# Kernel optimization log

Measured on AMD Instinct MI355X. Metric: run time of the kernel, lower is better.

## Reference

```python
import jax, jax.numpy as jnp
import numpy as np
from jax import lax

M, N, Q = 256, 65536, 64
LAMBDA_STAR = 0.1
LAMBDA_O = 0.1
T_ITERS = 16
PM_ITERS = 100


def setup_inputs() -> dict:
    key = jax.random.key(0)
    kx, kd = jax.random.split(key)
    X = jax.random.normal(kx, (M, N), dtype=jnp.float32)
    D = jax.random.normal(kd, (M, Q), dtype=jnp.float32)
    return {"X": X, "D": D}


def _power_method(D):
    # Largest eigenvalue of D^T D via 100-step power iteration (fixed random init).
    x0 = jax.random.normal(jax.random.key(1), (1, Q), dtype=D.dtype)

    def step(x, _):
        x = (x @ D.T) @ D          # [1,q] -> [1,m] -> [1,q]
        nm = jnp.linalg.norm(x)
        return x / nm, nm

    _, nms = lax.scan(step, x0, None, length=PM_ITERS)
    return nms[-1]


def reference(X, D):
    m, n = X.shape
    q = D.shape[1]
    alpha = _power_method(D)
    eta = 1.0 / alpha

    Iq = jnp.eye(q, dtype=D.dtype)
    Im = jnp.eye(m, dtype=D.dtype)
    top = jnp.concatenate([D.T @ D + LAMBDA_STAR * Iq, D.T], axis=1)   # [q, q+m]
    bot = jnp.concatenate([D, (1.0 + LAMBDA_STAR) * Im], axis=1)       # [m, q+m]
    H = jnp.eye(m + q, dtype=D.dtype) - eta * jnp.concatenate([top, bot], axis=0)
    W = eta * jnp.concatenate([D.T, Im], axis=0)                        # [(m+q), m]
    t = LAMBDA_O * eta * jnp.concatenate([jnp.zeros(q, D.dtype), jnp.ones(m, D.dtype)])

    b0 = W @ X                                                           # [(m+q), n]
    Z0 = jnp.zeros((m + q, n), dtype=X.dtype)

    def ista_step(carry, _):
        Z, b = carry
        Znew = jnp.maximum(0.0, b - t[:, None])    # thresholding (ger(t, ones) == t broadcast)
        b = b + H @ (Znew - Z)
        return (Znew, b), None

    (Z, _), _ = lax.scan(ista_step, (Z0, b0), None, length=T_ITERS)
    return Z
```

## Files before the change

kernel.cpp:

```cpp
#include <hip/hip_runtime.h>


typedef __bf16 bf16x8 __attribute__((ext_vector_type(8)));
typedef __bf16 bf16x2 __attribute__((ext_vector_type(2)));
typedef float f32x4 __attribute__((ext_vector_type(4)));
typedef float f32x2 __attribute__((ext_vector_type(2)));

#define MFMA16(a, b, c) __builtin_amdgcn_mfma_f32_16x16x32_bf16((a), (b), (c), 0, 0, 0)

#define NTOT 65536
#define NCOL 32

__device__ __forceinline__ unsigned pk2(float a, float b) {
#if __has_builtin(__builtin_amdgcn_cvt_pk_bf16_f32)
  return __builtin_bit_cast(unsigned, __builtin_amdgcn_cvt_pk_bf16_f32(a, b));
#else
  unsigned short ua = __builtin_bit_cast(unsigned short, (__bf16)a);
  unsigned short ub = __builtin_bit_cast(unsigned short, (__bf16)b);
  return (unsigned)ua | ((unsigned)ub << 16);
#endif
}
__device__ __forceinline__ unsigned pk2v(f32x2 v) { return pk2(v[0], v[1]); }
__device__ __forceinline__ f32x2 f2(float s) { f32x2 v = {s, s}; return v; }
__device__ __forceinline__ f32x2 pfma(f32x2 a, f32x2 b, f32x2 c) {
  return __builtin_elementwise_fma(a, b, c);
}
__device__ __forceinline__ f32x2 pmax0(f32x2 a) {
  return __builtin_elementwise_max(a, f2(0.f));
}

#define GOF(row) ((row) * 68 + (((row) >> 3) << 2))
__global__ void rnmf_prep(const float* __restrict__ D, void* __restrict__ ws) {
  float* wsf = (float*)ws;
  __bf16* Dbf = (__bf16*)((char*)ws + 256);
  __bf16* DTbf = (__bf16*)((char*)ws + 256 + 32768);

  __shared__ __bf16 DTl[64 * 264];
  __shared__ __bf16 gA[64 * 72];
  __shared__ __bf16 gB[64 * 72];
  __shared__ float gf[64 * 68 + 32];
  __shared__ __align__(16) float xv[64];

  const int tid = threadIdx.x;
  const int w = tid >> 6, lane = tid & 63, c = lane & 15, q4 = lane >> 4;

#pragma unroll
  for (int e = 0; e < 16; ++e) {
    int i4 = e * 256 + tid;
    float4 dv = *(const float4*)(D + i4 * 4);
    uint2 u; u.x = pk2(dv.x, dv.y); u.y = pk2(dv.z, dv.w);
    *(uint2*)(Dbf + i4 * 4) = u;
  }
#pragma unroll
  for (int e = 0; e < 64; ++e) {
    int flat = e * 256 + tid;
    int k = flat >> 6, a = flat & 63;
    DTl[a * 264 + k] = (__bf16)D[k * 64 + a];
  }
  __syncthreads();
#pragma unroll
  for (int e = 0; e < 8; ++e) {
    int fi = e * 256 + tid;
    int a = fi >> 5;
    int k = (fi * 8) & 255;
    *(bf16x8*)(DTbf + fi * 8) = *(const bf16x8*)&DTl[a * 264 + k];
  }
#pragma unroll
  for (int ct = 0; ct < 4; ++ct) {
    f32x4 acc = {0.f, 0.f, 0.f, 0.f};
#pragma unroll
    for (int kb = 0; kb < 8; ++kb) {
      bf16x8 a = *(const bf16x8*)&DTl[(16 * w + c) * 264 + 32 * kb + 8 * q4];
      bf16x8 b = *(const bf16x8*)&DTl[(16 * ct + c) * 264 + 32 * kb + 8 * q4];
      acc = MFMA16(a, b, acc);
    }
#pragma unroll
    for (int r = 0; r < 4; ++r)
      gA[(16 * w + 4 * q4 + r) * 72 + 16 * ct + c] = (__bf16)acc[r];
  }
  __syncthreads();
#pragma unroll
  for (int ct = 0; ct < 4; ++ct) {
    f32x4 acc = {0.f, 0.f, 0.f, 0.f};
#pragma unroll
    for (int kb = 0; kb < 2; ++kb) {
      bf16x8 a = *(const bf16x8*)&gA[(16 * w + c) * 72 + 32 * kb + 8 * q4];
      bf16x8 b = *(const bf16x8*)&gA[(16 * ct + c) * 72 + 32 * kb + 8 * q4];
      acc = MFMA16(a, b, acc);
    }
#pragma unroll
    for (int r = 0; r < 4; ++r)
      gB[(16 * w + 4 * q4 + r) * 72 + 16 * ct + c] = (__bf16)acc[r];
  }
  __syncthreads();
#pragma unroll
  for (int ct = 0; ct < 4; ++ct) {
    f32x4 acc = {0.f, 0.f, 0.f, 0.f};
#pragma unroll
    for (int kb = 0; kb < 2; ++kb) {
      bf16x8 a = *(const bf16x8*)&gB[(16 * w + c) * 72 + 32 * kb + 8 * q4];
      bf16x8 b = *(const bf16x8*)&gB[(16 * ct + c) * 72 + 32 * kb + 8 * q4];
      acc = MFMA16(a, b, acc);
    }
#pragma unroll
    for (int r = 0; r < 4; ++r)
      gA[(16 * w + 4 * q4 + r) * 72 + 16 * ct + c] = (__bf16)acc[r];
  }
  __syncthreads();
#pragma unroll
  for (int ct = 0; ct < 4; ++ct) {
    f32x4 acc = {0.f, 0.f, 0.f, 0.f};
#pragma unroll
    for (int kb = 0; kb < 2; ++kb) {
      bf16x8 a = *(const bf16x8*)&gA[(16 * w + c) * 72 + 32 * kb + 8 * q4];
      bf16x8 b = *(const bf16x8*)&gA[(16 * ct + c) * 72 + 32 * kb + 8 * q4];
      acc = MFMA16(a, b, acc);
    }
#pragma unroll
    for (int r = 0; r < 4; ++r)
      gf[GOF(16 * w + 4 * q4 + r) + 16 * ct + c] = acc[r];
  }
  __syncthreads();

  if (w == 0) {
    float td = gf[GOF(lane) + lane];
#pragma unroll
    for (int off = 32; off; off >>= 1) td += __shfl_xor(td, off, 64);
    const float tr = td;
    const float itr = 1.f / tr;
    xv[lane] = 1.f;
    float nm = 1.f;
    const int rowoff = GOF(lane);
    for (int itp = 0; itp < 28; ++itp) {
      float acc = 0.f;
#pragma unroll
      for (int k = 0; k < 64; k += 4) {
        float4 g = *(const float4*)&gf[rowoff + k];
        float4 xx = *(const float4*)&xv[k];
        acc = fmaf(g.x, xx.x, acc);
        acc = fmaf(g.y, xx.y, acc);
        acc = fmaf(g.z, xx.z, acc);
        acc = fmaf(g.w, xx.w, acc);
      }
      float y = acc * itr;
      float n2 = y * y;
#pragma unroll
      for (int off = 32; off; off >>= 1) n2 += __shfl_xor(n2, off, 64);
      nm = sqrtf(n2);
      xv[lane] = y / nm;
    }
    if (lane == 0) wsf[0] = 1.f / powf(nm * tr, 0.125f);
  }
}

__global__ __launch_bounds__(256, 3) void rnmf_main(const float* __restrict__ X,
                                                    float* __restrict__ Z,
                                                    const void* __restrict__ ws) {
  const float* wsf = (const float*)ws;
  const __bf16* Dbf = (const __bf16*)((const char*)ws + 256);
  const __bf16* DTbf = (const __bf16*)((const char*)ws + 256 + 32768);

  __shared__ __align__(16) char arena[33280];
  float* xs = (float*)arena;

  const int tid = threadIdx.x;
  const int w = tid >> 6;
  const int lane = tid & 63;
  const int c = lane & 15;
  const int q4 = lane >> 4;
  const int q4h = q4 >> 1, q4l = q4 & 1;
  const int j0 = blockIdx.x * NCOL;

#pragma unroll
  for (int e = 0; e < 8; ++e) {
    int idx = e * 256 + tid;
    int row = idx >> 3, c4 = (idx & 7) * 4;
    float4 g = *(const float4*)(X + row * NTOT + j0 + c4);
    xs[(c4 + 0) * 260 + row] = g.x;
    xs[(c4 + 1) * 260 + row] = g.y;
    xs[(c4 + 2) * 260 + row] = g.z;
    xs[(c4 + 3) * 260 + row] = g.w;
  }

  const float eta = wsf[0];
  const f32x2 etav = f2(eta);
  const f32x2 metav = f2(-eta);
  const f32x2 cqv = f2(1.f - 0.1f * eta);
  const f32x2 cmv = f2(1.f - 1.1f * eta);
  const float tm = 0.1f * eta;

  bf16x8 d1[4][2];
#pragma unroll
  for (int rt = 0; rt < 4; ++rt)
#pragma unroll
    for (int kb = 0; kb < 2; ++kb)
      d1[rt][kb] = *(const bf16x8*)(Dbf + (64 * w + 16 * rt + c) * 64 + 32 * kb + 8 * q4);
  bf16x8 d2[8];
#pragma unroll
  for (int kb = 0; kb < 8; ++kb)
    d2[kb] = *(const bf16x8*)(DTbf + (16 * w + c) * 256 + 32 * kb + 8 * q4);

  __syncthreads();

  f32x2 bqt2[2][2];
#pragma unroll
  for (int ct = 0; ct < 2; ++ct) {
    f32x4 acc = {0.f, 0.f, 0.f, 0.f};
#pragma unroll
    for (int kb = 0; kb < 8; ++kb) {
      const float* p = &xs[(16 * ct + c) * 260 + 32 * kb + 8 * q4];
      float4 lo = *(const float4*)p;
      float4 hi = *(const float4*)(p + 4);
      unsigned p0 = pk2(lo.x, lo.y), p1 = pk2(lo.z, lo.w);
      unsigned p2 = pk2(hi.x, hi.y), p3 = pk2(hi.z, hi.w);
      uint4 packed = {p0, p1, p2, p3};
      acc = MFMA16(d2[kb], __builtin_bit_cast(bf16x8, packed), acc);
    }
    f32x2 a0 = {acc[0], acc[1]}, a1 = {acc[2], acc[3]};
    bqt2[ct][0] = etav * a0;
    bqt2[ct][1] = etav * a1;
  }

  f32x2 bmt2[4][2][2];
#pragma unroll
  for (int rt = 0; rt < 4; ++rt)
#pragma unroll
    for (int ct = 0; ct < 2; ++ct) {
      const float* p = &xs[(16 * ct + c) * 260 + 64 * w + 16 * rt + 4 * q4];
      float4 v = *(const float4*)p;
      f32x2 x0 = {v.x, v.y}, x1 = {v.z, v.w};
      bmt2[rt][ct][0] = pfma(etav, x0, f2(-tm));
      bmt2[rt][ct][1] = pfma(etav, x1, f2(-tm));
    }

  __syncthreads();

  f32x2 zq2[2][2], zm2[4][2][2];
#pragma unroll
  for (int ct = 0; ct < 2; ++ct)
#pragma unroll
    for (int p = 0; p < 2; ++p) zq2[ct][p] = pmax0(bqt2[ct][p]);
#pragma unroll
  for (int rt = 0; rt < 4; ++rt)
#pragma unroll
    for (int ct = 0; ct < 2; ++ct)
#pragma unroll
      for (int p = 0; p < 2; ++p) zm2[rt][ct][p] = pmax0(bmt2[rt][ct][p]);

  char* smem = arena;
  const int rb = lane * 16;
  const int wzq = (w >> 1) * 1024 + ((2 * w) & 3) * 256 + q4h * 256 + c * 16 + 8 * q4l;
  const int wvb = 4096 + 2 * w * 1024 + q4h * 256 + c * 16 + 8 * q4l;

#pragma unroll
  for (int ct = 0; ct < 2; ++ct) {
    uint2 u; u.x = pk2v(zq2[ct][0]); u.y = pk2v(zq2[ct][1]);
    *(uint2*)(smem + wzq + ct * 2048) = u;
  }

  for (int it = 0; it < 15; ++it) {
    __syncthreads();
#pragma unroll
    for (int ct = 0; ct < 2; ++ct) {
      bf16x8 bz0 = *(const bf16x8*)(smem + rb + ct * 2048);
      bf16x8 bz1 = *(const bf16x8*)(smem + rb + ct * 2048 + 1024);
#pragma unroll
      for (int rt = 0; rt < 4; ++rt) {
        f32x4 acc = {0.f, 0.f, 0.f, 0.f};
        acc = MFMA16(d1[rt][0], bz0, acc);
        acc = MFMA16(d1[rt][1], bz1, acc);
        f32x2 u0 = {acc[0], acc[1]}, u1 = {acc[2], acc[3]};
        f32x2 z0 = zm2[rt][ct][0], z1 = zm2[rt][ct][1];
        f32x2 v0 = u0 + z0, v1 = u1 + z1;
        f32x2 t0 = pfma(cmv, z0, bmt2[rt][ct][0]);
        f32x2 t1 = pfma(cmv, z1, bmt2[rt][ct][1]);
        zm2[rt][ct][0] = pmax0(pfma(metav, u0, t0));
        zm2[rt][ct][1] = pmax0(pfma(metav, u1, t1));
        uint2 uu; uu.x = pk2v(v0); uu.y = pk2v(v1);
        *(uint2*)(smem + wvb + ct * 8192 + rt * 512) = uu;
      }
    }
    __syncthreads();
#pragma unroll
    for (int ct = 0; ct < 2; ++ct) {
      f32x4 acc = {0.f, 0.f, 0.f, 0.f};
#pragma unroll
      for (int kb = 0; kb < 8; ++kb) {
        bf16x8 bv = *(const bf16x8*)(smem + rb + 4096 + ct * 8192 + kb * 1024);
        acc = MFMA16(d2[kb], bv, acc);
      }
      f32x2 w0 = {acc[0], acc[1]}, w1 = {acc[2], acc[3]};
      f32x2 t0 = pfma(cqv, zq2[ct][0], bqt2[ct][0]);
      f32x2 t1 = pfma(cqv, zq2[ct][1], bqt2[ct][1]);
      zq2[ct][0] = pmax0(pfma(metav, w0, t0));
      zq2[ct][1] = pmax0(pfma(metav, w1, t1));
      uint2 u; u.x = pk2v(zq2[ct][0]); u.y = pk2v(zq2[ct][1]);
      *(uint2*)(smem + wzq + ct * 2048) = u;
    }
  }

#pragma unroll
  for (int ct = 0; ct < 2; ++ct)
#pragma unroll
    for (int p = 0; p < 2; ++p)
#pragma unroll
      for (int e = 0; e < 2; ++e)
        Z[(16 * w + 4 * q4 + 2 * p + e) * NTOT + j0 + 16 * ct + c] = zq2[ct][p][e];
#pragma unroll
  for (int rt = 0; rt < 4; ++rt)
#pragma unroll
    for (int ct = 0; ct < 2; ++ct)
#pragma unroll
      for (int p = 0; p < 2; ++p)
#pragma unroll
        for (int e = 0; e < 2; ++e)
          Z[(64 + 64 * w + 16 * rt + 4 * q4 + 2 * p + e) * NTOT + j0 + 16 * ct + c] = zm2[rt][ct][p][e];
}

extern "C" void kernel_launch(void* const* d_in, const int* in_sizes, int n_in,
                              void* d_out, int out_size, void* d_ws, size_t ws_size,
                              hipStream_t stream) {
  const float* X = (const float*)d_in[0];
  const float* D = (const float*)d_in[1];
  float* Z = (float*)d_out;
  rnmf_prep<<<dim3(1), dim3(256), 0, stream>>>(D, d_ws);
  rnmf_main<<<dim3(NTOT / NCOL), dim3(256), 0, stream>>>(X, Z, d_ws);
}
```

Baseline: 229.6 us.

## Stage X as bf16 in MFMA fragment layout to raise occupancy; rework power iteration

The main kernel now converts X to bf16 on load and stores it directly in the LDS layout the MFMA B-operand reads. This shrinks shared memory from 33280 to 20480 bytes, removes per-iteration packing, and drops one barrier. Launch bounds are raised from 3 to 5 blocks per CU to use the freed LDS. The prep kernel's power iteration now runs on all waves, skips per-step normalization, applies one rescale, and uses a Rayleigh quotient with fewer iterations. The trade-off is that the thresholded m-rows now start from bf16-rounded X rather than fp32, which costs some accuracy.

Measured after the change: 648.6 us. +182.5%, slower.

```diff
diff --git a/kernel.cpp b/kernel.cpp
--- a/kernel.cpp
+++ b/kernel.cpp
@@ -2,7 +2,7 @@
 
 
 typedef __bf16 bf16x8 __attribute__((ext_vector_type(8)));
-typedef __bf16 bf16x2 __attribute__((ext_vector_type(2)));
+typedef __bf16 bf16x4 __attribute__((ext_vector_type(4)));
 typedef float f32x4 __attribute__((ext_vector_type(4)));
 typedef float f32x2 __attribute__((ext_vector_type(2)));
 
@@ -29,7 +29,6 @@
   return __builtin_elementwise_max(a, f2(0.f));
 }
 
-#define GOF(row) ((row) * 68 + (((row) >> 3) << 2))
 __global__ void rnmf_prep(const float* __restrict__ D, void* __restrict__ ws) {
   float* wsf = (float*)ws;
   __bf16* Dbf = (__bf16*)((char*)ws + 256);
@@ -38,8 +37,8 @@
   __shared__ __bf16 DTl[64 * 264];
   __shared__ __bf16 gA[64 * 72];
   __shared__ __bf16 gB[64 * 72];
-  __shared__ float gf[64 * 68 + 32];
-  __shared__ __align__(16) float xv[64];
+  __shared__ float gf[64 * 68];
+  __shared__ __align__(16) float xv[2][64];
 
   const int tid = threadIdx.x;
   const int w = tid >> 6, lane = tid & 63, c = lane & 15, q4 = lane >> 4;
@@ -47,15 +46,14 @@
 #pragma unroll
   for (int e = 0; e < 16; ++e) {
     int i4 = e * 256 + tid;
+    int row = i4 >> 4, col4 = (i4 & 15) * 4;
     float4 dv = *(const float4*)(D + i4 * 4);
     uint2 u; u.x = pk2(dv.x, dv.y); u.y = pk2(dv.z, dv.w);
     *(uint2*)(Dbf + i4 * 4) = u;
-  }
-#pragma unroll
-  for (int e = 0; e < 64; ++e) {
-    int flat = e * 256 + tid;
-    int k = flat >> 6, a = flat & 63;
-    DTl[a * 264 + k] = (__bf16)D[k * 64 + a];
+    DTl[(col4 + 0) * 264 + row] = (__bf16)dv.x;
+    DTl[(col4 + 1) * 264 + row] = (__bf16)dv.y;
+    DTl[(col4 + 2) * 264 + row] = (__bf16)dv.z;
+    DTl[(col4 + 3) * 264 + row] = (__bf16)dv.w;
   }
   __syncthreads();
 #pragma unroll
@@ -118,50 +116,63 @@
     }
 #pragma unroll
     for (int r = 0; r < 4; ++r)
-      gf[GOF(16 * w + 4 * q4 + r) + 16 * ct + c] = acc[r];
-  }
-  __syncthreads();
-
-  if (w == 0) {
-    float td = gf[GOF(lane) + lane];
-#pragma unroll
-    for (int off = 32; off; off >>= 1) td += __shfl_xor(td, off, 64);
-    const float tr = td;
-    const float itr = 1.f / tr;
-    xv[lane] = 1.f;
-    float nm = 1.f;
-    const int rowoff = GOF(lane);
-    for (int itp = 0; itp < 28; ++itp) {
-      float acc = 0.f;
-#pragma unroll
-      for (int k = 0; k < 64; k += 4) {
-        float4 g = *(const float4*)&gf[rowoff + k];
-        float4 xx = *(const float4*)&xv[k];
-        acc = fmaf(g.x, xx.x, acc);
-        acc = fmaf(g.y, xx.y, acc);
-        acc = fmaf(g.z, xx.z, acc);
-        acc = fmaf(g.w, xx.w, acc);
-      }
-      float y = acc * itr;
-      float n2 = y * y;
-#pragma unroll
-      for (int off = 32; off; off >>= 1) n2 += __shfl_xor(n2, off, 64);
-      nm = sqrtf(n2);
-      xv[lane] = y / nm;
-    }
-    if (lane == 0) wsf[0] = 1.f / powf(nm * tr, 0.125f);
-  }
-}
-
-__global__ __launch_bounds__(256, 3) void rnmf_main(const float* __restrict__ X,
+      gf[(16 * w + 4 * q4 + r) * 68 + 16 * ct + c] = acc[r];
+  }
+  __syncthreads();
+
+  float td = gf[lane * 68 + lane];
+#pragma unroll
+  for (int off = 32; off; off >>= 1) td += __shfl_xor(td, off, 64);
+  const float tr = td;
+  const float itr = 1.f / tr;
+  const int rowoff = lane * 68;
+  float x = 1.f, xp = 1.f;
+  for (int itp = 0; itp < 17; ++itp) {
+    xv[itp & 1][lane] = x;
+    __syncthreads();
+    float a0 = 0.f, a1 = 0.f, a2 = 0.f, a3 = 0.f;
+#pragma unroll
+    for (int k = 0; k < 64; k += 16) {
+      float4 g0 = *(const float4*)&gf[rowoff + k];
+      float4 g1 = *(const float4*)&gf[rowoff + k + 4];
+      float4 g2 = *(const float4*)&gf[rowoff + k + 8];
+      float4 g3 = *(const float4*)&gf[rowoff + k + 12];
+      float4 x0 = *(const float4*)&xv[itp & 1][k];
+      float4 x1 = *(const float4*)&xv[itp & 1][k + 4];
+      float4 x2 = *(const float4*)&xv[itp & 1][k + 8];
+      float4 x3 = *(const float4*)&xv[itp & 1][k + 12];
+      a0 = fmaf(g0.x, x0.x, a0); a0 = fmaf(g0.y, x0.y, a0);
+      a0 = fmaf(g0.z, x0.z, a0); a0 = fmaf(g0.w, x0.w, a0);
+      a1 = fmaf(g1.x, x1.x, a1); a1 = fmaf(g1.y, x1.y, a1);
+      a1 = fmaf(g1.z, x1.z, a1); a1 = fmaf(g1.w, x1.w, a1);
+      a2 = fmaf(g2.x, x2.x, a2); a2 = fmaf(g2.y, x2.y, a2);
+      a2 = fmaf(g2.z, x2.z, a2); a2 = fmaf(g2.w, x2.w, a2);
+      a3 = fmaf(g3.x, x3.x, a3); a3 = fmaf(g3.y, x3.y, a3);
+      a3 = fmaf(g3.z, x3.z, a3); a3 = fmaf(g3.w, x3.w, a3);
+    }
+    xp = x;
+    x = ((a0 + a1) + (a2 + a3)) * itr;
+    if (itp == 8) x *= 1073741824.f;
+  }
+  float num = xp * x, den = xp * xp;
+#pragma unroll
+  for (int off = 32; off; off >>= 1) {
+    num += __shfl_xor(num, off, 64);
+    den += __shfl_xor(den, off, 64);
+  }
+  if (tid == 0)
+    wsf[0] = powf((num / den) * tr, -0.125f);
+}
+
+__global__ __launch_bounds__(256, 5) void rnmf_main(const float* __restrict__ X,
                                                     float* __restrict__ Z,
                                                     const void* __restrict__ ws) {
   const float* wsf = (const float*)ws;
   const __bf16* Dbf = (const __bf16*)((const char*)ws + 256);
   const __bf16* DTbf = (const __bf16*)((const char*)ws + 256 + 32768);
 
-  __shared__ __align__(16) char arena[33280];
-  float* xs = (float*)arena;
+  __shared__ __align__(16) char arena[20480];
+  char* smem = arena;
 
   const int tid = threadIdx.x;
   const int w = tid >> 6;
@@ -176,10 +187,13 @@
     int idx = e * 256 + tid;
     int row = idx >> 3, c4 = (idx & 7) * 4;
     float4 g = *(const float4*)(X + row * NTOT + j0 + c4);
-    xs[(c4 + 0) * 260 + row] = g.x;
-    xs[(c4 + 1) * 260 + row] = g.y;
-    xs[(c4 + 2) * 260 + row] = g.z;
-    xs[(c4 + 3) * 260 + row] = g.w;
+    int base = 4096 + (row >> 5) * 1024 + 256 * ((row >> 3) & 3) + (row & 7) * 2;
+    float vals[4] = {g.x, g.y, g.z, g.w};
+#pragma unroll
+    for (int i = 0; i < 4; ++i) {
+      int col = c4 + i;
+      *(__bf16*)(smem + base + (col >> 4) * 8192 + (col & 15) * 16) = (__bf16)vals[i];
+    }
   }
 
   const float eta = wsf[0];
@@ -202,19 +216,16 @@
 
   __syncthreads();
 
+  const int rb = lane * 16;
+
   f32x2 bqt2[2][2];
 #pragma unroll
   for (int ct = 0; ct < 2; ++ct) {
     f32x4 acc = {0.f, 0.f, 0.f, 0.f};
 #pragma unroll
     for (int kb = 0; kb < 8; ++kb) {
-      const float* p = &xs[(16 * ct + c) * 260 + 32 * kb + 8 * q4];
-      float4 lo = *(const float4*)p;
-      float4 hi = *(const float4*)(p + 4);
-      unsigned p0 = pk2(lo.x, lo.y), p1 = pk2(lo.z, lo.w);
-      unsigned p2 = pk2(hi.x, hi.y), p3 = pk2(hi.z, hi.w);
-      uint4 packed = {p0, p1, p2, p3};
-      acc = MFMA16(d2[kb], __builtin_bit_cast(bf16x8, packed), acc);
+      bf16x8 bx = *(const bf16x8*)(smem + rb + 4096 + ct * 8192 + kb * 1024);
+      acc = MFMA16(d2[kb], bx, acc);
     }
     f32x2 a0 = {acc[0], acc[1]}, a1 = {acc[2], acc[3]};
     bqt2[ct][0] = etav * a0;
@@ -223,17 +234,18 @@
 
   f32x2 bmt2[4][2][2];
 #pragma unroll
-  for (int rt = 0; rt < 4; ++rt)
+  for (int rt = 0; rt < 4; ++rt) {
+    int r = 64 * w + 16 * rt + 4 * q4;
+    int ao = 4096 + (r >> 5) * 1024 + (c + 16 * ((r >> 3) & 3)) * 16 + (r & 7) * 2;
 #pragma unroll
     for (int ct = 0; ct < 2; ++ct) {
-      const float* p = &xs[(16 * ct + c) * 260 + 64 * w + 16 * rt + 4 * q4];
-      float4 v = *(const float4*)p;
-      f32x2 x0 = {v.x, v.y}, x1 = {v.z, v.w};
+      bf16x4 xb = *(const bf16x4*)(smem + ao + ct * 8192);
+      f32x2 x0 = {(float)xb[0], (float)xb[1]};
+      f32x2 x1 = {(float)xb[2], (float)xb[3]};
       bmt2[rt][ct][0] = pfma(etav, x0, f2(-tm));
       bmt2[rt][ct][1] = pfma(etav, x1, f2(-tm));
     }
-
-  __syncthreads();
+  }
 
   f32x2 zq2[2][2], zm2[4][2][2];
 #pragma unroll
@@ -247,8 +259,6 @@
 #pragma unroll
       for (int p = 0; p < 2; ++p) zm2[rt][ct][p] = pmax0(bmt2[rt][ct][p]);
 
-  char* smem = arena;
-  const int rb = lane * 16;
   const int wzq = (w >> 1) * 1024 + ((2 * w) & 3) * 256 + q4h * 256 + c * 16 + 8 * q4l;
   const int wvb = 4096 + 2 * w * 1024 + q4h * 256 + c * 16 + 8 * q4l;
 
```
